# Kernel optimization log

Measured on AMD Instinct MI355X. Metric: run time of the kernel, lower is better.

## Reference

```python
import jax, jax.numpy as jnp
import numpy as np

H, W = 96, 96
NUM_ITERS = 5          # num_iterations from __init__
SXY_G, COMPAT_G = 3.0, 3.0    # addPairwiseGaussian(sxy=(3,3), compat=3)
SXY_B, SRGB, COMPAT_B = 50.0, 20.0, 10.0  # addPairwiseBilateral(sxy=50, srgb=20, compat=10)
EPS = 1e-8


def _crf_marginals(img, m):
    """Exact dense mean-field CRF (the math pydensecrf approximates via
    permutohedral lattice). img: [H,W] float, m: [H,W] int in {0,1}.
    Returns Q: [2, N] marginals."""
    Hh, Ww = img.shape
    N = Hh * Ww
    # --- unary (replicates the source exactly, including the label swap) ---
    onehot0 = (m == 0).astype(jnp.float32)
    unary_p = jnp.stack([1.0 - onehot0, onehot0]).reshape(2, -1)   # [2, N]
    unary = -jnp.log(jnp.clip(unary_p, EPS, 1.0))
    # --- pairwise kernel: 3 * gaussian + 10 * bilateral, self-excluded ---
    ys, xs = jnp.meshgrid(jnp.arange(Hh, dtype=jnp.float32),
                          jnp.arange(Ww, dtype=jnp.float32), indexing='ij')
    pos = jnp.stack([xs.ravel(), ys.ravel()], axis=-1)             # [N, 2]
    f = img.reshape(-1)                                            # [N]
    d2 = jnp.sum((pos[:, None, :] - pos[None, :, :]) ** 2, axis=-1)  # [N, N] spatial sq dist
    # grayscale image duplicated into 2 feature channels -> 2 * (f_i - f_j)^2
    df2 = 2.0 * (f[:, None] - f[None, :]) ** 2                     # [N, N]
    K = (COMPAT_G * jnp.exp(-d2 / (2.0 * SXY_G ** 2))
         + COMPAT_B * jnp.exp(-d2 / (2.0 * SXY_B ** 2) - df2 / (2.0 * SRGB ** 2)))
    idx = jnp.arange(N)
    K = K.at[idx, idx].set(0.0)  # exclude self-interaction
    # --- mean-field iterations (Potts compatibility, 2 labels) ---
    Q = jax.nn.softmax(-unary, axis=0)  # [2, N]
    for _ in range(NUM_ITERS):
        msg = Q @ K                     # [2, N]; K is symmetric
        pairwise = msg[::-1]            # Potts: penalty from the OTHER label
        Q = jax.nn.softmax(-unary - pairwise, axis=0)
    return Q


def setup_inputs() -> dict:
    key = jax.random.key(0)
    k1, k2 = jax.random.split(key)
    image = jax.random.uniform(k1, (1, 1, H, W), dtype=jnp.float32) * 255.0
    mask = jax.random.randint(k2, (1, 1, H, W), 0, 2)
    return {"image": image, "mask": mask}


def reference(image, mask):
    img = image[0, 0]
    m = mask[0, 0]
    Q = _crf_marginals(img, m)
    pred = jnp.argmax(Q, axis=0).reshape(img.shape)
    return pred[None, None].astype(jnp.float32)   # [1,1,H,W]
```

## Files before the change

### kernel.cpp

```cpp
#include <hip/hip_runtime.h>

constexpr int W    = 96;
constexpr int NPIX = 9216;
constexpr int NM   = 31;
constexpr int NPKB = 16;
constexpr int NP   = 17;

constexpr float LCLIP = 18.420681f;

__global__ __launch_bounds__(256) void k_init(const float* __restrict__ img,
                                              float4* __restrict__ B4){
    int px = blockIdx.x*256 + threadIdx.x;
    float th = img[px] * 0.0122718463f;
    float c[64];
    c[0] = 1.f; c[63] = 0.f;
    float s1, c1;
    sincosf(th, &s1, &c1);
    float cm = 1.f, sm = 0.f;
    #pragma unroll
    for (int m = 1; m <= NM; ++m){
        float cn = cm*c1 - sm*s1;
        float sn = sm*c1 + cm*s1;
        cm = cn; sm = sn;
        c[m]    = cm;
        c[NM+m] = sm;
    }
    #pragma unroll
    for (int p = 0; p < NPKB; ++p)
        B4[(size_t)p*NPIX + px] = make_float4(c[4*p], c[4*p+1], c[4*p+2], c[4*p+3]);
}

template<int MODE>
__global__ __launch_bounds__(384) void k_H(const int* __restrict__ mask,
        const float4* __restrict__ B4,
        const float* __restrict__ partV, const float* __restrict__ partVk,
        float* __restrict__ ksum, const float* __restrict__ qprev, float* __restrict__ qcur,
        float4* __restrict__ H4T, float* __restrict__ H3T,
        float4* __restrict__ H4Tk, float* __restrict__ H3Tk)
{
    __shared__ float4 P4[8*97];
    __shared__ float  qp[8*97];
    __shared__ float  tw[193];
    const int  t    = threadIdx.x;
    const int  B    = blockIdx.x;
    const int  g0   = blockIdx.y;
    const bool ones = (MODE==0) && (g0 >= NP);
    const int  pack = ones ? g0 - NP : g0;
    const bool G3   = (pack == NPKB);

    if (t < 193){
        float d = (float)(t - 96);
        tw[t] = G3 ? __expf(-d*d*(1.f/18.f)) : __expf(-d*d*(1.f/5000.f));
    }
    float A[4];
    if (!G3){
        #pragma unroll
        for (int jj = 0; jj < 4; ++jj){
            int cch = 4*pack + jj;
            if (cch == 0)       A[jj] = 0.6923648f;
            else if (cch <= 62){
                int m = (cch <= NM) ? cch : cch - NM;
                A[jj] = 1.3847296f * __expf(-0.0150598f*(float)(m*m));
            } else              A[jj] = 0.f;
        }
    }

    #pragma unroll
    for (int k = 0; k < 2; ++k){
        int l  = t + k*384;
        int px = B*768 + l;
        float q;
        if (ones){
            q = 1.f;
        } else if (MODE == 0){
            q = (mask[px]==0) ? 1.f/(1.f+__expf( LCLIP)) : 1.f/(1.f+__expf(-LCLIP));
        } else {
            float m = 0.f;
            #pragma unroll
            for (int p = 0; p < NP; ++p) m += partV[(size_t)p*NPIX + px];
            float kk;
            if (MODE == 1){
                kk = 0.f;
                #pragma unroll
                for (int p = 0; p < NP; ++p) kk += partVk[(size_t)p*NPIX + px];
                kk -= 13.f;
                if (g0 == 0) ksum[px] = kk;
            } else {
                kk = ksum[px];
            }
            float duv = (mask[px]==0) ? LCLIP : -LCLIP;
            float delta = duv + kk - 2.f*(m - 13.f*qprev[px]);
            q = 1.f/(1.f+__expf(delta));
        }
        if (!ones && g0 == 0) qcur[px] = q;
        int ryl = l/96, xx = l - ryl*96;
        if (!G3){
            float4 b = B4[(size_t)pack*NPIX + px];
            P4[ryl*97 + xx] = make_float4(q*A[0]*b.x, q*A[1]*b.y, q*A[2]*b.z, q*A[3]*b.w);
        } else {
            qp[ryl*97 + xx] = q;
        }
    }
    __syncthreads();

    const int r = t & 7, xg = t >> 3;
    const int y = 8*B + r;
    if (!G3){
        float4 a0 = make_float4(0.f,0.f,0.f,0.f), a1 = a0;
        #pragma unroll 4
        for (int xp = 0; xp < W; ++xp){
            float4 v  = P4[r*97 + xp];
            float  w0 = tw[xg - xp + 96];
            float  w1 = tw[xg - xp + 96 + 48];
            a0.x = fmaf(w0,v.x,a0.x); a0.y = fmaf(w0,v.y,a0.y);
            a0.z = fmaf(w0,v.z,a0.z); a0.w = fmaf(w0,v.w,a0.w);
            a1.x = fmaf(w1,v.x,a1.x); a1.y = fmaf(w1,v.y,a1.y);
            a1.z = fmaf(w1,v.z,a1.z); a1.w = fmaf(w1,v.w,a1.w);
        }
        float4* dst = ones ? H4Tk : H4T;
        dst[(size_t)pack*NPIX + xg*W      + y] = a0;
        dst[(size_t)pack*NPIX + (xg+48)*W + y] = a1;
    } else {
        float h0 = 0.f, h1 = 0.f;
        #pragma unroll 4
        for (int xp = 0; xp < W; ++xp){
            float qv = qp[r*97 + xp];
            h0 = fmaf(tw[xg - xp + 96],      qv, h0);
            h1 = fmaf(tw[xg - xp + 96 + 48], qv, h1);
        }
        float* dg = ones ? H3Tk : H3T;
        dg[xg*W + y] = h0; dg[(xg+48)*W + y] = h1;
    }
}

__global__ __launch_bounds__(384) void k_V(const float4* __restrict__ B4,
        const float4* __restrict__ H4T, const float4* __restrict__ H4Tk,
        const float* __restrict__ H3T, const float* __restrict__ H3Tk,
        float* __restrict__ partV, float* __restrict__ partVk)
{
    __shared__ float4 Hl[8*97];
    __shared__ float  Hl3[8*97];
    __shared__ float  tw[193];
    const int  t    = threadIdx.x;
    const int  C    = blockIdx.x;
    const int  g0   = blockIdx.y;
    const bool ones = g0 >= NP;
    const int  pack = ones ? g0 - NP : g0;
    const bool G3   = (pack == NPKB);

    if (t < 193){
        float d = (float)(t - 96);
        tw[t] = G3 ? __expf(-d*d*(1.f/18.f)) : __expf(-d*d*(1.f/5000.f));
    }
    #pragma unroll
    for (int k = 0; k < 2; ++k){
        int l = t + k*384;
        int col = l/96, yy = l - col*96;
        if (!G3) Hl[col*97 + yy]  = (ones ? H4Tk : H4T)[(size_t)pack*NPIX + (8*C+col)*W + yy];
        else     Hl3[col*97 + yy] = (ones ? H3Tk : H3T)[(8*C+col)*W + yy];
    }
    __syncthreads();

    const int r = t & 7, yg = t >> 3;
    const int x = 8*C + r;
    if (!G3){
        float4 a0 = make_float4(0.f,0.f,0.f,0.f), a1 = a0;
        #pragma unroll 4
        for (int yp = 0; yp < W; ++yp){
            float4 v  = Hl[r*97 + yp];
            float  w0 = tw[yg - yp + 96];
            float  w1 = tw[yg - yp + 96 + 48];
            a0.x = fmaf(w0,v.x,a0.x); a0.y = fmaf(w0,v.y,a0.y);
            a0.z = fmaf(w0,v.z,a0.z); a0.w = fmaf(w0,v.w,a0.w);
            a1.x = fmaf(w1,v.x,a1.x); a1.y = fmaf(w1,v.y,a1.y);
            a1.z = fmaf(w1,v.z,a1.z); a1.w = fmaf(w1,v.w,a1.w);
        }
        int px0 = yg*W + x, px1 = (yg+48)*W + x;
        float4 b0 = B4[(size_t)pack*NPIX + px0];
        float4 b1 = B4[(size_t)pack*NPIX + px1];
        float* dst = ones ? partVk : partV;
        dst[(size_t)pack*NPIX + px0] = a0.x*b0.x + a0.y*b0.y + a0.z*b0.z + a0.w*b0.w;
        dst[(size_t)pack*NPIX + px1] = a1.x*b1.x + a1.y*b1.y + a1.z*b1.z + a1.w*b1.w;
    } else {
        float h0 = 0.f, h1 = 0.f;
        #pragma unroll 4
        for (int yp = 0; yp < W; ++yp){
            float v = Hl3[r*97 + yp];
            h0 = fmaf(tw[yg - yp + 96],      v, h0);
            h1 = fmaf(tw[yg - yp + 96 + 48], v, h1);
        }
        float* dst = ones ? partVk : partV;
        dst[(size_t)pack*NPIX + yg*W + x]      = 3.f*h0;
        dst[(size_t)pack*NPIX + (yg+48)*W + x] = 3.f*h1;
    }
}

__global__ __launch_bounds__(256) void k_F(const int* __restrict__ mask,
        const float* __restrict__ partV, const float* __restrict__ ksum,
        const float* __restrict__ qprev, float* __restrict__ out){
    int px = blockIdx.x*256 + threadIdx.x;
    float m = 0.f;
    #pragma unroll
    for (int p = 0; p < NP; ++p) m += partV[(size_t)p*NPIX + px];
    float duv = (mask[px]==0) ? LCLIP : -LCLIP;
    float delta = duv + ksum[px] - 2.f*(m - 13.f*qprev[px]);
    out[px] = (delta > 0.f) ? 1.f : 0.f;
}

extern "C" void kernel_launch(void* const* d_in, const int* in_sizes, int n_in,
                              void* d_out, int out_size, void* d_ws, size_t ws_size,
                              hipStream_t stream){
    const float* img  = (const float*)d_in[0];
    const int*   mask = (const int*)d_in[1];
    float* out = (float*)d_out;
    float* ws  = (float*)d_ws;

    constexpr size_t TBL = (size_t)NPKB*NPIX*4;
    float4* B4    = (float4*)ws;
    float4* H4T   = (float4*)(ws + TBL);
    float4* H4Tk  = (float4*)(ws + 2*TBL);
    float*  base  = ws + 3*TBL;
    float* H3T   = base;
    float* H3Tk  = H3T  + NPIX;
    float* partV = H3Tk + NPIX;
    float* partVk= partV + (size_t)NP*NPIX;
    float* qA    = partVk + (size_t)NP*NPIX;
    float* qB    = qA + NPIX;
    float* ksum  = qB + NPIX;

    dim3 b(384);
    k_init<<<dim3(36), dim3(256), 0, stream>>>(img, B4);
    k_H<0><<<dim3(12,2*NP), b, 0, stream>>>(mask, B4, partV, partVk, ksum, qA, qA, H4T, H3T, H4Tk, H3Tk);
    k_V   <<<dim3(12,2*NP), b, 0, stream>>>(B4, H4T, H4Tk, H3T, H3Tk, partV, partVk);
    k_H<1><<<dim3(12,NP), b, 0, stream>>>(mask, B4, partV, partVk, ksum, qA, qB, H4T, H3T, H4Tk, H3Tk);
    k_V   <<<dim3(12,NP), b, 0, stream>>>(B4, H4T, H4Tk, H3T, H3Tk, partV, partVk);
    k_H<2><<<dim3(12,NP), b, 0, stream>>>(mask, B4, partV, partVk, ksum, qB, qA, H4T, H3T, H4Tk, H3Tk);
    k_V   <<<dim3(12,NP), b, 0, stream>>>(B4, H4T, H4Tk, H3T, H3Tk, partV, partVk);
    k_H<2><<<dim3(12,NP), b, 0, stream>>>(mask, B4, partV, partVk, ksum, qA, qB, H4T, H3T, H4Tk, H3Tk);
    k_V   <<<dim3(12,NP), b, 0, stream>>>(B4, H4T, H4Tk, H3T, H3Tk, partV, partVk);
    k_H<2><<<dim3(12,NP), b, 0, stream>>>(mask, B4, partV, partVk, ksum, qB, qA, H4T, H3T, H4Tk, H3Tk);
    k_V   <<<dim3(12,NP), b, 0, stream>>>(B4, H4T, H4Tk, H3T, H3Tk, partV, partVk);
    k_F<<<dim3(36), dim3(256), 0, stream>>>(mask, partV, ksum, qA, out);
}
```

Before: 80.67 us.

## Fuse cosine/sine basis init into first H pass and halve block size

Removes the separate k_init launch. The first horizontal pass now computes each pixel's cos/sin harmonic basis inline through a sincos recurrence, writes it to the B4 table for later passes, and uses it directly. The H and V kernels drop from 384 to 192 threads per block, and each thread now produces four outputs instead of two. This cuts one kernel launch and its global round trip, but adds redundant recurrence work in every pack block of the first pass and lowers per-block thread parallelism.

```diff
diff --git a/kernel.cpp b/kernel.cpp
--- a/kernel.cpp
+++ b/kernel.cpp
@@ -7,32 +7,11 @@
 constexpr int NP   = 17;
 
 constexpr float LCLIP = 18.420681f;
-
-__global__ __launch_bounds__(256) void k_init(const float* __restrict__ img,
-                                              float4* __restrict__ B4){
-    int px = blockIdx.x*256 + threadIdx.x;
-    float th = img[px] * 0.0122718463f;
-    float c[64];
-    c[0] = 1.f; c[63] = 0.f;
-    float s1, c1;
-    sincosf(th, &s1, &c1);
-    float cm = 1.f, sm = 0.f;
-    #pragma unroll
-    for (int m = 1; m <= NM; ++m){
-        float cn = cm*c1 - sm*s1;
-        float sn = sm*c1 + cm*s1;
-        cm = cn; sm = sn;
-        c[m]    = cm;
-        c[NM+m] = sm;
-    }
-    #pragma unroll
-    for (int p = 0; p < NPKB; ++p)
-        B4[(size_t)p*NPIX + px] = make_float4(c[4*p], c[4*p+1], c[4*p+2], c[4*p+3]);
-}
+constexpr float K512  = 0.0122718463f;
 
 template<int MODE>
-__global__ __launch_bounds__(384) void k_H(const int* __restrict__ mask,
-        const float4* __restrict__ B4,
+__global__ __launch_bounds__(192) void k_H(const float* __restrict__ img,
+        const int* __restrict__ mask, float4* __restrict__ B4,
         const float* __restrict__ partV, const float* __restrict__ partVk,
         float* __restrict__ ksum, const float* __restrict__ qprev, float* __restrict__ qcur,
         float4* __restrict__ H4T, float* __restrict__ H3T,
@@ -56,18 +35,18 @@
     if (!G3){
         #pragma unroll
         for (int jj = 0; jj < 4; ++jj){
-            int cch = 4*pack + jj;
-            if (cch == 0)       A[jj] = 0.6923648f;
-            else if (cch <= 62){
-                int m = (cch <= NM) ? cch : cch - NM;
+            int ch = 4*pack + jj;
+            if (ch == 0)       A[jj] = 0.6923648f;
+            else if (ch <= 62){
+                int m = (ch <= NM) ? ch : ch - NM;
                 A[jj] = 1.3847296f * __expf(-0.0150598f*(float)(m*m));
-            } else              A[jj] = 0.f;
+            } else             A[jj] = 0.f;
         }
     }
 
     #pragma unroll
-    for (int k = 0; k < 2; ++k){
-        int l  = t + k*384;
+    for (int k = 0; k < 4; ++k){
+        int l  = t + k*192;
         int px = B*768 + l;
         float q;
         if (ones){
@@ -95,8 +74,32 @@
         if (!ones && g0 == 0) qcur[px] = q;
         int ryl = l/96, xx = l - ryl*96;
         if (!G3){
-            float4 b = B4[(size_t)pack*NPIX + px];
-            P4[ryl*97 + xx] = make_float4(q*A[0]*b.x, q*A[1]*b.y, q*A[2]*b.z, q*A[3]*b.w);
+            float cv0, cv1, cv2, cv3;
+            if (MODE == 0){
+                float cv[4];
+                #pragma unroll
+                for (int jj = 0; jj < 4; ++jj) cv[jj] = (4*pack+jj == 0) ? 1.f : 0.f;
+                float s1, c1;
+                sincosf(img[px]*K512, &s1, &c1);
+                float cm = 1.f, sm = 0.f;
+                for (int m = 1; m <= NM; ++m){
+                    float cn = cm*c1 - sm*s1;
+                    float sn = sm*c1 + cm*s1;
+                    cm = cn; sm = sn;
+                    #pragma unroll
+                    for (int jj = 0; jj < 4; ++jj){
+                        int ch = 4*pack + jj;
+                        int mm = (ch <= NM) ? ch : ch - NM;
+                        if (ch >= 1 && ch <= 62 && mm == m) cv[jj] = (ch <= NM) ? cm : sm;
+                    }
+                }
+                cv0=cv[0]; cv1=cv[1]; cv2=cv[2]; cv3=cv[3];
+                if (!ones) B4[(size_t)pack*NPIX + px] = make_float4(cv0,cv1,cv2,cv3);
+            } else {
+                float4 b = B4[(size_t)pack*NPIX + px];
+                cv0=b.x; cv1=b.y; cv2=b.z; cv3=b.w;
+            }
+            P4[ryl*97 + xx] = make_float4(q*A[0]*cv0, q*A[1]*cv1, q*A[2]*cv2, q*A[3]*cv3);
         } else {
             qp[ryl*97 + xx] = q;
         }
@@ -106,34 +109,47 @@
     const int r = t & 7, xg = t >> 3;
     const int y = 8*B + r;
     if (!G3){
-        float4 a0 = make_float4(0.f,0.f,0.f,0.f), a1 = a0;
+        float4 a0 = make_float4(0.f,0.f,0.f,0.f), a1 = a0, a2 = a0, a3 = a0;
         #pragma unroll 4
         for (int xp = 0; xp < W; ++xp){
             float4 v  = P4[r*97 + xp];
-            float  w0 = tw[xg - xp + 96];
-            float  w1 = tw[xg - xp + 96 + 48];
+            int    i0 = xg - xp + 96;
+            float  w0 = tw[i0],      w1 = tw[i0+24];
+            float  w2 = tw[i0+48],   w3 = tw[i0+72];
             a0.x = fmaf(w0,v.x,a0.x); a0.y = fmaf(w0,v.y,a0.y);
             a0.z = fmaf(w0,v.z,a0.z); a0.w = fmaf(w0,v.w,a0.w);
             a1.x = fmaf(w1,v.x,a1.x); a1.y = fmaf(w1,v.y,a1.y);
             a1.z = fmaf(w1,v.z,a1.z); a1.w = fmaf(w1,v.w,a1.w);
-        }
-        float4* dst = ones ? H4Tk : H4T;
-        dst[(size_t)pack*NPIX + xg*W      + y] = a0;
-        dst[(size_t)pack*NPIX + (xg+48)*W + y] = a1;
+            a2.x = fmaf(w2,v.x,a2.x); a2.y = fmaf(w2,v.y,a2.y);
+            a2.z = fmaf(w2,v.z,a2.z); a2.w = fmaf(w2,v.w,a2.w);
+            a3.x = fmaf(w3,v.x,a3.x); a3.y = fmaf(w3,v.y,a3.y);
+            a3.z = fmaf(w3,v.z,a3.z); a3.w = fmaf(w3,v.w,a3.w);
+        }
+        float4* dst = (ones ? H4Tk : H4T) + (size_t)pack*NPIX + y;
+        dst[(xg     )*W] = a0;
+        dst[(xg + 24)*W] = a1;
+        dst[(xg + 48)*W] = a2;
+        dst[(xg + 72)*W] = a3;
     } else {
-        float h0 = 0.f, h1 = 0.f;
+        float h0=0.f, h1=0.f, h2=0.f, h3=0.f;
         #pragma unroll 4
         for (int xp = 0; xp < W; ++xp){
             float qv = qp[r*97 + xp];
-            h0 = fmaf(tw[xg - xp + 96],      qv, h0);
-            h1 = fmaf(tw[xg - xp + 96 + 48], qv, h1);
-        }
-        float* dg = ones ? H3Tk : H3T;
-        dg[xg*W + y] = h0; dg[(xg+48)*W + y] = h1;
-    }
-}
-
-__global__ __launch_bounds__(384) void k_V(const float4* __restrict__ B4,
+            int   i0 = xg - xp + 96;
+            h0 = fmaf(tw[i0],    qv, h0);
+            h1 = fmaf(tw[i0+24], qv, h1);
+            h2 = fmaf(tw[i0+48], qv, h2);
+            h3 = fmaf(tw[i0+72], qv, h3);
+        }
+        float* dg = (ones ? H3Tk : H3T) + y;
+        dg[(xg     )*W] = h0;
+        dg[(xg + 24)*W] = h1;
+        dg[(xg + 48)*W] = h2;
+        dg[(xg + 72)*W] = h3;
+    }
+}
+
+__global__ __launch_bounds__(192) void k_V(const float4* __restrict__ B4,
         const float4* __restrict__ H4T, const float4* __restrict__ H4Tk,
         const float* __restrict__ H3T, const float* __restrict__ H3Tk,
         float* __restrict__ partV, float* __restrict__ partVk)
@@ -153,8 +169,8 @@
         tw[t] = G3 ? __expf(-d*d*(1.f/18.f)) : __expf(-d*d*(1.f/5000.f));
     }
     #pragma unroll
-    for (int k = 0; k < 2; ++k){
-        int l = t + k*384;
+    for (int k = 0; k < 4; ++k){
+        int l = t + k*192;
         int col = l/96, yy = l - col*96;
         if (!G3) Hl[col*97 + yy]  = (ones ? H4Tk : H4T)[(size_t)pack*NPIX + (8*C+col)*W + yy];
         else     Hl3[col*97 + yy] = (ones ? H3Tk : H3T)[(8*C+col)*W + yy];
@@ -164,34 +180,46 @@
     const int r = t & 7, yg = t >> 3;
     const int x = 8*C + r;
     if (!G3){
-        float4 a0 = make_float4(0.f,0.f,0.f,0.f), a1 = a0;
+        float4 a0 = make_float4(0.f,0.f,0.f,0.f), a1 = a0, a2 = a0, a3 = a0;
         #pragma unroll 4
         for (int yp = 0; yp < W; ++yp){
             float4 v  = Hl[r*97 + yp];
-            float  w0 = tw[yg - yp + 96];
-            float  w1 = tw[yg - yp + 96 + 48];
+            int    i0 = yg - yp + 96;
+            float  w0 = tw[i0],    w1 = tw[i0+24];
+            float  w2 = tw[i0+48], w3 = tw[i0+72];
             a0.x = fmaf(w0,v.x,a0.x); a0.y = fmaf(w0,v.y,a0.y);
             a0.z = fmaf(w0,v.z,a0.z); a0.w = fmaf(w0,v.w,a0.w);
             a1.x = fmaf(w1,v.x,a1.x); a1.y = fmaf(w1,v.y,a1.y);
             a1.z = fmaf(w1,v.z,a1.z); a1.w = fmaf(w1,v.w,a1.w);
-        }
-        int px0 = yg*W + x, px1 = (yg+48)*W + x;
-        float4 b0 = B4[(size_t)pack*NPIX + px0];
-        float4 b1 = B4[(size_t)pack*NPIX + px1];
+            a2.x = fmaf(w2,v.x,a2.x); a2.y = fmaf(w2,v.y,a2.y);
+            a2.z = fmaf(w2,v.z,a2.z); a2.w = fmaf(w2,v.w,a2.w);
+            a3.x = fmaf(w3,v.x,a3.x); a3.y = fmaf(w3,v.y,a3.y);
+            a3.z = fmaf(w3,v.z,a3.z); a3.w = fmaf(w3,v.w,a3.w);
+        }
         float* dst = ones ? partVk : partV;
-        dst[(size_t)pack*NPIX + px0] = a0.x*b0.x + a0.y*b0.y + a0.z*b0.z + a0.w*b0.w;
-        dst[(size_t)pack*NPIX + px1] = a1.x*b1.x + a1.y*b1.y + a1.z*b1.z + a1.w*b1.w;
+        #pragma unroll
+        for (int o = 0; o < 4; ++o){
+            float4 a = (o==0)?a0:(o==1)?a1:(o==2)?a2:a3;
+            int px = (yg + 24*o)*W + x;
+            float4 b = B4[(size_t)pack*NPIX + px];
+            dst[(size_t)pack*NPIX + px] = a.x*b.x + a.y*b.y + a.z*b.z + a.w*b.w;
+        }
     } else {
-        float h0 = 0.f, h1 = 0.f;
+        float h0=0.f, h1=0.f, h2=0.f, h3=0.f;
         #pragma unroll 4
         for (int yp = 0; yp < W; ++yp){
             float v = Hl3[r*97 + yp];
-            h0 = fmaf(tw[yg - yp + 96],      v, h0);
-            h1 = fmaf(tw[yg - yp + 96 + 48], v, h1);
-        }
-        float* dst = ones ? partVk : partV;
-        dst[(size_t)pack*NPIX + yg*W + x]      = 3.f*h0;
-        dst[(size_t)pack*NPIX + (yg+48)*W + x] = 3.f*h1;
+            int  i0 = yg - yp + 96;
+            h0 = fmaf(tw[i0],    v, h0);
+            h1 = fmaf(tw[i0+24], v, h1);
+            h2 = fmaf(tw[i0+48], v, h2);
+            h3 = fmaf(tw[i0+72], v, h3);
+        }
+        float* dst = (ones ? partVk : partV) + (size_t)pack*NPIX + x;
+        dst[(yg     )*W] = 3.f*h0;
+        dst[(yg + 24)*W] = 3.f*h1;
+        dst[(yg + 48)*W] = 3.f*h2;
+        dst[(yg + 72)*W] = 3.f*h3;
     }
 }
 
@@ -228,17 +256,16 @@
     float* qB    = qA + NPIX;
     float* ksum  = qB + NPIX;
 
-    dim3 b(384);
-    k_init<<<dim3(36), dim3(256), 0, stream>>>(img, B4);
-    k_H<0><<<dim3(12,2*NP), b, 0, stream>>>(mask, B4, partV, partVk, ksum, qA, qA, H4T, H3T, H4Tk, H3Tk);
+    dim3 b(192);
+    k_H<0><<<dim3(12,2*NP), b, 0, stream>>>(img, mask, B4, partV, partVk, ksum, qA, qA, H4T, H3T, H4Tk, H3Tk);
     k_V   <<<dim3(12,2*NP), b, 0, stream>>>(B4, H4T, H4Tk, H3T, H3Tk, partV, partVk);
-    k_H<1><<<dim3(12,NP), b, 0, stream>>>(mask, B4, partV, partVk, ksum, qA, qB, H4T, H3T, H4Tk, H3Tk);
-    k_V   <<<dim3(12,NP), b, 0, stream>>>(B4, H4T, H4Tk, H3T, H3Tk, partV, partVk);
-    k_H<2><<<dim3(12,NP), b, 0, stream>>>(mask, B4, partV, partVk, ksum, qB, qA, H4T, H3T, H4Tk, H3Tk);
-    k_V   <<<dim3(12,NP), b, 0, stream>>>(B4, H4T, H4Tk, H3T, H3Tk, partV, partVk);
-    k_H<2><<<dim3(12,NP), b, 0, stream>>>(mask, B4, partV, partVk, ksum, qA, qB, H4T, H3T, H4Tk, H3Tk);
-    k_V   <<<dim3(12,NP), b, 0, stream>>>(B4, H4T, H4Tk, H3T, H3Tk, partV, partVk);
-    k_H<2><<<dim3(12,NP), b, 0, stream>>>(mask, B4, partV, partVk, ksum, qB, qA, H4T, H3T, H4Tk, H3Tk);
+    k_H<1><<<dim3(12,NP), b, 0, stream>>>(img, mask, B4, partV, partVk, ksum, qA, qB, H4T, H3T, H4Tk, H3Tk);
+    k_V   <<<dim3(12,NP), b, 0, stream>>>(B4, H4T, H4Tk, H3T, H3Tk, partV, partVk);
+    k_H<2><<<dim3(12,NP), b, 0, stream>>>(img, mask, B4, partV, partVk, ksum, qB, qA, H4T, H3T, H4Tk, H3Tk);
+    k_V   <<<dim3(12,NP), b, 0, stream>>>(B4, H4T, H4Tk, H3T, H3Tk, partV, partVk);
+    k_H<2><<<dim3(12,NP), b, 0, stream>>>(img, mask, B4, partV, partVk, ksum, qA, qB, H4T, H3T, H4Tk, H3Tk);
+    k_V   <<<dim3(12,NP), b, 0, stream>>>(B4, H4T, H4Tk, H3T, H3Tk, partV, partVk);
+    k_H<2><<<dim3(12,NP), b, 0, stream>>>(img, mask, B4, partV, partVk, ksum, qB, qA, H4T, H3T, H4Tk, H3Tk);
     k_V   <<<dim3(12,NP), b, 0, stream>>>(B4, H4T, H4Tk, H3T, H3Tk, partV, partVk);
     k_F<<<dim3(36), dim3(256), 0, stream>>>(mask, partV, ksum, qA, out);
 }
```

Result: slower. 102.5 us (+27.1%).
